# Kernel tuning notes

Hardware: AMD Instinct MI355X
Metric: run time of the kernel (lower is better)

Reference implementation:

```python
import jax, jax.numpy as jnp
import numpy as np

K = 8192  # num_embeddings
D = 256   # embedding_dim


def setup_inputs() -> dict:
    key = jax.random.key(0)
    k1, k2 = jax.random.split(key)
    z_e = jax.random.normal(k1, (16, 2048, D), dtype=jnp.float32)
    # codebook init: randn * 1/sqrt(D), matching the torch buffer init
    embedding = jax.random.normal(k2, (K, D), dtype=jnp.float32) * (1.0 / np.sqrt(D))
    return {"z_e": z_e, "embedding": embedding}


def reference(z_e, embedding):
    # Eval-mode forward of VectorQuantizerEMA (no EMA buffer update, no mask).
    B, M, Dd = z_e.shape
    Kk = embedding.shape[0]
    flat = z_e.reshape(-1, Dd)  # [N, D]

    distances = (
        jnp.sum(flat * flat, axis=1, keepdims=True)
        - 2.0 * (flat @ embedding.T)
        + jnp.sum(embedding * embedding, axis=1)[None, :]
    )
    indices = jnp.argmin(distances, axis=1)  # [N] int

    z_q = embedding[indices].reshape(B, M, Dd)
    z_q_st = z_e + jax.lax.stop_gradient(z_q - z_e)

    # instantaneous usage stats (perplexity, dead ratio)
    usage = jnp.zeros((Kk,), dtype=jnp.float32).at[indices].add(1.0)
    total = jnp.maximum(usage.sum(), 1.0)
    probs = usage / total
    safe_p = jnp.where(probs > 0, probs, 1.0)
    perplexity = jnp.exp(-jnp.sum(probs * jnp.log(safe_p)))
    dead_ratio = jnp.mean((usage == 0).astype(jnp.float32))
    stats = jnp.stack([perplexity, dead_ratio])

    return z_q_st, z_q, indices.reshape(B, M), stats
```

## Files before the change

### kernel.cpp

```cpp
#include <hip/hip_runtime.h>

#define N_ROWS 32768
#define D_DIM  256
#define K_CODES 8192

#define OUT0_OFF 0
#define OUT1_OFF 8388608
#define OUTI_OFF 16777216
#define OUTS_OFF 16809984

typedef _Float16 half4 __attribute__((ext_vector_type(4)));
typedef _Float16 half8 __attribute__((ext_vector_type(8)));
typedef float    f32x16 __attribute__((ext_vector_type(16)));

#define HN_OFF  0x400000
#define CAND_OFF 0x500000

#define MARGIN 0.05f

__global__ __launch_bounds__(256) void vq_conv_e(const float* __restrict__ E,
                                                 char* __restrict__ Estg,
                                                 float* __restrict__ hn,
                                                 int* __restrict__ usage) {
    const int wv = threadIdx.x >> 6;
    const int l = threadIdx.x & 63;
    const int code = blockIdx.x * 4 + wv;
    float4 v = ((const float4*)E)[code * 64 + l];

    const int g = code >> 6, c = code & 63;
    const int st = l >> 5;
    const int dg = ((4 * l) & 127) >> 3;
    const int slot = (dg + c) & 15;
    const int sub = 8 * (l & 1);

    half4 hh = {(_Float16)v.x, (_Float16)v.y, (_Float16)v.z, (_Float16)v.w};
    char* p = Estg + (size_t)g * 32768 + st * 16384 + c * 256 + slot * 16 + sub;
    *(half4*)p = hh;

    float s = v.x * v.x + v.y * v.y + v.z * v.z + v.w * v.w;
    #pragma unroll
    for (int off = 32; off >= 1; off >>= 1) s += __shfl_down(s, off);
    if (l == 0) hn[code] = -0.5f * s;

    if (blockIdx.x < K_CODES / 256) usage[blockIdx.x * 256 + threadIdx.x] = 0;
}

__global__ __launch_bounds__(256) void vq_conv_x(const float* __restrict__ x,
                                                 char* __restrict__ Xh) {
    const size_t i4 = ((size_t)blockIdx.x * 256 + threadIdx.x) * 4;
    float4 v = *(const float4*)(x + i4);
    half4 hh = {(_Float16)v.x, (_Float16)v.y, (_Float16)v.z, (_Float16)v.w};
    *(half4*)(Xh + i4 * 2) = hh;
}

#define STAGE_COMPUTE(LDSOFF, KSB)                                             \
    _Pragma("unroll")                                                          \
    for (int ks = 0; ks < 8; ++ks) {                                           \
        const int slot = (2 * ks + hc) & 15;                                   \
        const int sa = rb0 + slot * 16 + (LDSOFF);                             \
        half8 a0 = *(const half8*)(lds + sa);                                  \
        half8 a1 = *(const half8*)(lds + sa + 8192);                           \
        const half8 b0 = xr0[(KSB) + ks];                                      \
        const half8 b1 = xr1[(KSB) + ks];                                      \
        acc00 = __builtin_amdgcn_mfma_f32_32x32x16_f16(a0, b0, acc00, 0, 0, 0);\
        acc01 = __builtin_amdgcn_mfma_f32_32x32x16_f16(a0, b1, acc01, 0, 0, 0);\
        acc10 = __builtin_amdgcn_mfma_f32_32x32x16_f16(a1, b0, acc10, 0, 0, 0);\
        acc11 = __builtin_amdgcn_mfma_f32_32x32x16_f16(a1, b1, acc11, 0, 0, 0);\
    }

#define ISSUE_STAGE(gsrc, BUFOFF)                                              \
    _Pragma("unroll") for (int i = 0; i < 4; ++i)                              \
        __builtin_amdgcn_global_load_lds(                                      \
            (const __attribute__((address_space(1))) void*)((gsrc) + i * 4096 + t16), \
            (__attribute__((address_space(3))) void*)(lds + (BUFOFF) + i * 4096 + t16), \
            16, 0, 0);

#define TOP2_UPD(v, cidx, T0, T1, I0, I1)                                      \
    if ((v) > (T1)) {                                                          \
        const bool g_ = (v) > (T0);                                            \
        (T1) = g_ ? (T0) : (v);                                                \
        (I1) = g_ ? (I0) : (cidx);                                             \
        if (g_) { (T0) = (v); (I0) = (cidx); }                                 \
    }

__global__ __launch_bounds__(256, 2) void vq_mfma(const char* __restrict__ Estg,
                                                  const float* __restrict__ hnp,
                                                  const char* __restrict__ Xh,
                                                  float2* __restrict__ cand) {
    __shared__ __attribute__((aligned(16))) char lds[32768];

    const int tid = threadIdx.x;
    const int w = tid >> 6, lane = tid & 63;
    const int cl = lane & 31, half = lane >> 5;
    const int t16 = tid * 16;
    const int rb0 = cl * 256;
    const int hc = half + cl;

    const int part = blockIdx.x & 3;
    const int qb = blockIdx.x >> 2;
    const char* Ebase = Estg + (size_t)part * 32 * 32768;

    const int qw = qb * 256 + w * 64;
    const char* xbA = Xh + (size_t)(qw + cl) * 512 + half * 16;
    const char* xbB = Xh + (size_t)(qw + 32 + cl) * 512 + half * 16;
    half8 xr0[16], xr1[16];
    #pragma unroll
    for (int ks = 0; ks < 16; ++ks) {
        xr0[ks] = *(const half8*)(xbA + ks * 32);
        xr1[ks] = *(const half8*)(xbB + ks * 32);
    }

    ISSUE_STAGE(Ebase, 0)

    float t0a = -3.4e38f, t1a = -3.4e38f, t0b = -3.4e38f, t1b = -3.4e38f;
    int i0a = 0, i1a = 0, i0b = 0, i1b = 0;

    for (int g = 0; g < 32; ++g) {
        const char* egrp = Ebase + (size_t)g * 32768;
        const char* enxt = Ebase + (size_t)((g + 1) & 31) * 32768;

        f32x16 acc00 = {}, acc01 = {}, acc10 = {}, acc11 = {};

        __syncthreads();
        ISSUE_STAGE(egrp + 16384, 16384)
        const float* hq = hnp + part * 2048 + g * 64 + 4 * half;
        float4 hn0[4], hn1[4];
        #pragma unroll
        for (int j = 0; j < 4; ++j) {
            hn0[j] = *(const float4*)(hq + 8 * j);
            hn1[j] = *(const float4*)(hq + 32 + 8 * j);
        }
        STAGE_COMPUTE(0, 0)

        __syncthreads();
        ISSUE_STAGE(enxt, 0)
        STAGE_COMPUTE(16384, 8)

        const int gb = g * 64 + 4 * half;
        #pragma unroll
        for (int r = 0; r < 16; ++r) {
            const int rc = (r & 3) + 8 * (r >> 2);
            const float h0 = hn0[r >> 2][r & 3];
            const float h1 = hn1[r >> 2][r & 3];
            const int c0 = gb + rc, c1 = gb + 32 + rc;
            float v;
            v = acc00[r] + h0; TOP2_UPD(v, c0, t0a, t1a, i0a, i1a);
            v = acc10[r] + h1; TOP2_UPD(v, c1, t0a, t1a, i0a, i1a);
            v = acc01[r] + h0; TOP2_UPD(v, c0, t0b, t1b, i0b, i1b);
            v = acc11[r] + h1; TOP2_UPD(v, c1, t0b, t1b, i0b, i1b);
        }
    }

    const size_t bA = (size_t)(qw + cl) * 16 + part * 4 + half * 2;
    cand[bA]     = make_float2(t0a, __int_as_float(part * 2048 + i0a));
    cand[bA + 1] = make_float2(t1a, __int_as_float(part * 2048 + i1a));
    const size_t bB = (size_t)(qw + 32 + cl) * 16 + part * 4 + half * 2;
    cand[bB]     = make_float2(t0b, __int_as_float(part * 2048 + i0b));
    cand[bB + 1] = make_float2(t1b, __int_as_float(part * 2048 + i1b));
}

__global__ __launch_bounds__(64) void vq_resolve(const float2* __restrict__ cand,
                                                 const float* __restrict__ x,
                                                 const float* __restrict__ E,
                                                 float* __restrict__ outI,
                                                 int* __restrict__ wsIdx,
                                                 int* __restrict__ usage) {
    const int row = blockIdx.x;
    const int lane = threadIdx.x;

    float v = -3.4e38f;
    int ci = 0x7fffffff;
    if (lane < 16) {
        float2 c = cand[(size_t)row * 16 + lane];
        v = c.x;
        ci = __float_as_int(c.y);
    }
    float m = v;
    #pragma unroll
    for (int off = 8; off >= 1; off >>= 1) m = fmaxf(m, __shfl_xor(m, off, 16));
    m = __shfl(m, 0);

    const bool im = (lane < 16) && (v >= m - MARGIN);
    const unsigned long long mk = __ballot(im);
    int besti;
    if (__popcll(mk) == 1) {
        int wmin = im ? ci : 0x7fffffff;
        #pragma unroll
        for (int off = 8; off >= 1; off >>= 1)
            wmin = min(wmin, __shfl_xor(wmin, off, 16));
        besti = __shfl(wmin, 0);
    } else {
        const float4 x4 = *(const float4*)(x + (size_t)row * 256 + lane * 4);
        double bq = -1.0e300;
        besti = 0x7fffffff;
        unsigned long long mm = mk;
        while (mm) {
            const int j = __ffsll(mm) - 1;
            mm &= mm - 1;
            const int cidx = __shfl(ci, j);
            const float4 e4 = *(const float4*)(E + (size_t)cidx * 256 + lane * 4);
            double ps = (double)x4.x * e4.x + (double)x4.y * e4.y +
                        (double)x4.z * e4.z + (double)x4.w * e4.w -
                        0.5 * ((double)e4.x * e4.x + (double)e4.y * e4.y +
                               (double)e4.z * e4.z + (double)e4.w * e4.w);
            #pragma unroll
            for (int off = 32; off >= 1; off >>= 1) ps += __shfl_xor(ps, off);
            if (ps > bq || (ps == bq && cidx < besti)) { bq = ps; besti = cidx; }
        }
    }

    if (lane == 0) {
        outI[row] = (float)besti;
        wsIdx[row] = besti;
        atomicAdd(&usage[besti], 1);
    }
}

__global__ __launch_bounds__(64) void vq_gather(const int* __restrict__ wsIdx,
                                                const float* __restrict__ E,
                                                float* __restrict__ out0,
                                                float* __restrict__ out1) {
    const int row = blockIdx.x;
    const int lane = threadIdx.x;
    const int idx = wsIdx[row];
    float4 e4 = ((const float4*)(E + (size_t)idx * D_DIM))[lane];
    ((float4*)(out0 + (size_t)row * D_DIM))[lane] = e4;
    ((float4*)(out1 + (size_t)row * D_DIM))[lane] = e4;
}

__global__ __launch_bounds__(256) void vq_stats(const int* __restrict__ usage,
                                                float* __restrict__ statsOut) {
    __shared__ float redp[256];
    __shared__ int   redz[256];
    const int t = threadIdx.x;
    float pl = 0.0f;
    int zc = 0;
    for (int i = t; i < K_CODES; i += 256) {
        const int u = usage[i];
        if (u == 0) {
            zc++;
        } else {
            const float p = (float)u * (1.0f / (float)N_ROWS);
            pl += p * logf(p);
        }
    }
    redp[t] = pl;
    redz[t] = zc;
    __syncthreads();
    for (int s = 128; s > 0; s >>= 1) {
        if (t < s) { redp[t] += redp[t + s]; redz[t] += redz[t + s]; }
        __syncthreads();
    }
    if (t == 0) {
        statsOut[0] = expf(-redp[0]);
        statsOut[1] = (float)redz[0] / (float)K_CODES;
    }
}

extern "C" void kernel_launch(void* const* d_in, const int* in_sizes, int n_in,
                              void* d_out, int out_size, void* d_ws, size_t ws_size,
                              hipStream_t stream) {
    const float* z_e = (const float*)d_in[0];
    const float* E   = (const float*)d_in[1];

    float* out   = (float*)d_out;
    char*  out_b = (char*)d_out;

    char*   Estg  = out_b;
    float*  hn    = (float*)(out_b + HN_OFF);
    float2* candb = (float2*)(out_b + CAND_OFF);
    char*   Xh    = out_b + (size_t)OUT1_OFF * 4;

    float* out0 = out + OUT0_OFF;
    float* out1 = out + OUT1_OFF;
    float* outI = out + OUTI_OFF;
    float* outS = out + OUTS_OFF;

    int* usage = (int*)d_ws;
    int* wsIdx = (int*)((char*)d_ws + 32768);

    vq_conv_e<<<dim3(K_CODES / 4), dim3(256), 0, stream>>>(E, Estg, hn, usage);
    vq_conv_x<<<dim3(8192), dim3(256), 0, stream>>>(z_e, Xh);
    vq_mfma<<<dim3(512), dim3(256), 0, stream>>>(Estg, hn, Xh, candb);
    vq_resolve<<<dim3(N_ROWS), dim3(64), 0, stream>>>(candb, z_e, E, outI, wsIdx, usage);
    vq_gather<<<dim3(N_ROWS), dim3(64), 0, stream>>>(wsIdx, E, out0, out1);
    vq_stats<<<dim3(1), dim3(256), 0, stream>>>(usage, outS);
}
```

Measured before the change: 285.2 us.

## Fuse conversion kernels, pack group ids into low mantissa bits for argmax, widen blocks

The two conversion kernels are merged into one launch. In the MFMA kernel, the per-element top-2 tracking in the hot loop is replaced by a per-register running max: the group id is packed into the low 6 mantissa bits so fmaxf carries the index. Top-2 selection is done once after the loop. The resolve, gather and stats kernels get larger blocks with several rows per block. The packing drops precision in the low bits and keeps only one candidate per accumulator slot, which leans on the resolve margin to stay correct.

```diff
diff --git a/kernel.cpp b/kernel.cpp
--- a/kernel.cpp
+++ b/kernel.cpp
@@ -18,39 +18,42 @@
 
 #define MARGIN 0.05f
 
-__global__ __launch_bounds__(256) void vq_conv_e(const float* __restrict__ E,
-                                                 char* __restrict__ Estg,
-                                                 float* __restrict__ hn,
-                                                 int* __restrict__ usage) {
-    const int wv = threadIdx.x >> 6;
-    const int l = threadIdx.x & 63;
-    const int code = blockIdx.x * 4 + wv;
-    float4 v = ((const float4*)E)[code * 64 + l];
-
-    const int g = code >> 6, c = code & 63;
-    const int st = l >> 5;
-    const int dg = ((4 * l) & 127) >> 3;
-    const int slot = (dg + c) & 15;
-    const int sub = 8 * (l & 1);
-
-    half4 hh = {(_Float16)v.x, (_Float16)v.y, (_Float16)v.z, (_Float16)v.w};
-    char* p = Estg + (size_t)g * 32768 + st * 16384 + c * 256 + slot * 16 + sub;
-    *(half4*)p = hh;
-
-    float s = v.x * v.x + v.y * v.y + v.z * v.z + v.w * v.w;
-    #pragma unroll
-    for (int off = 32; off >= 1; off >>= 1) s += __shfl_down(s, off);
-    if (l == 0) hn[code] = -0.5f * s;
-
-    if (blockIdx.x < K_CODES / 256) usage[blockIdx.x * 256 + threadIdx.x] = 0;
-}
-
-__global__ __launch_bounds__(256) void vq_conv_x(const float* __restrict__ x,
-                                                 char* __restrict__ Xh) {
-    const size_t i4 = ((size_t)blockIdx.x * 256 + threadIdx.x) * 4;
-    float4 v = *(const float4*)(x + i4);
-    half4 hh = {(_Float16)v.x, (_Float16)v.y, (_Float16)v.z, (_Float16)v.w};
-    *(half4*)(Xh + i4 * 2) = hh;
+#define PK(v, id) __uint_as_float((__float_as_uint(v) & 0xFFFFFFC0u) | (unsigned)(id))
+
+__global__ __launch_bounds__(256) void vq_conv(const float* __restrict__ E,
+                                               const float* __restrict__ x,
+                                               char* __restrict__ Estg,
+                                               float* __restrict__ hn,
+                                               char* __restrict__ Xh,
+                                               int* __restrict__ usage) {
+    if (blockIdx.x < 2048) {
+        const int wv = threadIdx.x >> 6;
+        const int l = threadIdx.x & 63;
+        const int code = blockIdx.x * 4 + wv;
+        float4 v = ((const float4*)E)[code * 64 + l];
+
+        const int g = code >> 6, c = code & 63;
+        const int st = l >> 5;
+        const int dg = ((4 * l) & 127) >> 3;
+        const int slot = (dg + c) & 15;
+        const int sub = 8 * (l & 1);
+
+        half4 hh = {(_Float16)v.x, (_Float16)v.y, (_Float16)v.z, (_Float16)v.w};
+        char* p = Estg + (size_t)g * 32768 + st * 16384 + c * 256 + slot * 16 + sub;
+        *(half4*)p = hh;
+
+        float s = v.x * v.x + v.y * v.y + v.z * v.z + v.w * v.w;
+        #pragma unroll
+        for (int off = 32; off >= 1; off >>= 1) s += __shfl_down(s, off);
+        if (l == 0) hn[code] = -0.5f * s;
+
+        if (blockIdx.x < K_CODES / 256) usage[blockIdx.x * 256 + threadIdx.x] = 0;
+    } else {
+        const size_t i4 = ((size_t)(blockIdx.x - 2048) * 256 + threadIdx.x) * 4;
+        float4 v = *(const float4*)(x + i4);
+        half4 hh = {(_Float16)v.x, (_Float16)v.y, (_Float16)v.z, (_Float16)v.w};
+        *(half4*)(Xh + i4 * 2) = hh;
+    }
 }
 
 #define STAGE_COMPUTE(LDSOFF, KSB)                                             \
@@ -112,8 +115,9 @@
 
     ISSUE_STAGE(Ebase, 0)
 
-    float t0a = -3.4e38f, t1a = -3.4e38f, t0b = -3.4e38f, t1b = -3.4e38f;
-    int i0a = 0, i1a = 0, i0b = 0, i1b = 0;
+    float mA[16], mB[16];
+    #pragma unroll
+    for (int r = 0; r < 16; ++r) { mA[r] = -3.4e38f; mB[r] = -3.4e38f; }
 
     for (int g = 0; g < 32; ++g) {
         const char* egrp = Ebase + (size_t)g * 32768;
@@ -136,18 +140,36 @@
         ISSUE_STAGE(enxt, 0)
         STAGE_COMPUTE(16384, 8)
 
-        const int gb = g * 64 + 4 * half;
+        const int gid2 = g * 2;
         #pragma unroll
         for (int r = 0; r < 16; ++r) {
-            const int rc = (r & 3) + 8 * (r >> 2);
             const float h0 = hn0[r >> 2][r & 3];
             const float h1 = hn1[r >> 2][r & 3];
-            const int c0 = gb + rc, c1 = gb + 32 + rc;
-            float v;
-            v = acc00[r] + h0; TOP2_UPD(v, c0, t0a, t1a, i0a, i1a);
-            v = acc10[r] + h1; TOP2_UPD(v, c1, t0a, t1a, i0a, i1a);
-            v = acc01[r] + h0; TOP2_UPD(v, c0, t0b, t1b, i0b, i1b);
-            v = acc11[r] + h1; TOP2_UPD(v, c1, t0b, t1b, i0b, i1b);
+            mA[r] = fmaxf(fmaxf(mA[r], PK(acc00[r] + h0, gid2)),
+                          PK(acc10[r] + h1, gid2 + 1));
+            mB[r] = fmaxf(fmaxf(mB[r], PK(acc01[r] + h0, gid2)),
+                          PK(acc11[r] + h1, gid2 + 1));
+        }
+    }
+
+    float t0a = -3.4e38f, t1a = -3.4e38f, t0b = -3.4e38f, t1b = -3.4e38f;
+    int i0a = 0, i1a = 0, i0b = 0, i1b = 0;
+    #pragma unroll
+    for (int r = 0; r < 16; ++r) {
+        const int rc = (r & 3) + 8 * (r >> 2);
+        {
+            const unsigned b = __float_as_uint(mA[r]);
+            const int id = (int)(b & 63u);
+            const int code = (id >> 1) * 64 + (id & 1) * 32 + 4 * half + rc;
+            const float v = mA[r];
+            TOP2_UPD(v, code, t0a, t1a, i0a, i1a);
+        }
+        {
+            const unsigned b = __float_as_uint(mB[r]);
+            const int id = (int)(b & 63u);
+            const int code = (id >> 1) * 64 + (id & 1) * 32 + 4 * half + rc;
+            const float v = mB[r];
+            TOP2_UPD(v, code, t0b, t1b, i0b, i1b);
         }
     }
 
@@ -159,14 +181,14 @@
     cand[bB + 1] = make_float2(t1b, __int_as_float(part * 2048 + i1b));
 }
 
-__global__ __launch_bounds__(64) void vq_resolve(const float2* __restrict__ cand,
-                                                 const float* __restrict__ x,
-                                                 const float* __restrict__ E,
-                                                 float* __restrict__ outI,
-                                                 int* __restrict__ wsIdx,
-                                                 int* __restrict__ usage) {
-    const int row = blockIdx.x;
-    const int lane = threadIdx.x;
+__global__ __launch_bounds__(256) void vq_resolve(const float2* __restrict__ cand,
+                                                  const float* __restrict__ x,
+                                                  const float* __restrict__ E,
+                                                  float* __restrict__ outI,
+                                                  int* __restrict__ wsIdx,
+                                                  int* __restrict__ usage) {
+    const int row = blockIdx.x * 4 + (threadIdx.x >> 6);
+    const int lane = threadIdx.x & 63;
 
     float v = -3.4e38f;
     int ci = 0x7fffffff;
@@ -216,26 +238,26 @@
     }
 }
 
-__global__ __launch_bounds__(64) void vq_gather(const int* __restrict__ wsIdx,
-                                                const float* __restrict__ E,
-                                                float* __restrict__ out0,
-                                                float* __restrict__ out1) {
-    const int row = blockIdx.x;
-    const int lane = threadIdx.x;
+__global__ __launch_bounds__(256) void vq_gather(const int* __restrict__ wsIdx,
+                                                 const float* __restrict__ E,
+                                                 float* __restrict__ out0,
+                                                 float* __restrict__ out1) {
+    const int row = blockIdx.x * 4 + (threadIdx.x >> 6);
+    const int lane = threadIdx.x & 63;
     const int idx = wsIdx[row];
     float4 e4 = ((const float4*)(E + (size_t)idx * D_DIM))[lane];
     ((float4*)(out0 + (size_t)row * D_DIM))[lane] = e4;
     ((float4*)(out1 + (size_t)row * D_DIM))[lane] = e4;
 }
 
-__global__ __launch_bounds__(256) void vq_stats(const int* __restrict__ usage,
-                                                float* __restrict__ statsOut) {
-    __shared__ float redp[256];
-    __shared__ int   redz[256];
+__global__ __launch_bounds__(1024) void vq_stats(const int* __restrict__ usage,
+                                                 float* __restrict__ statsOut) {
+    __shared__ float redp[1024];
+    __shared__ int   redz[1024];
     const int t = threadIdx.x;
     float pl = 0.0f;
     int zc = 0;
-    for (int i = t; i < K_CODES; i += 256) {
+    for (int i = t; i < K_CODES; i += 1024) {
         const int u = usage[i];
         if (u == 0) {
             zc++;
@@ -247,7 +269,7 @@
     redp[t] = pl;
     redz[t] = zc;
     __syncthreads();
-    for (int s = 128; s > 0; s >>= 1) {
+    for (int s = 512; s > 0; s >>= 1) {
         if (t < s) { redp[t] += redp[t + s]; redz[t] += redz[t + s]; }
         __syncthreads();
     }
@@ -279,10 +301,9 @@
     int* usage = (int*)d_ws;
     int* wsIdx = (int*)((char*)d_ws + 32768);
 
-    vq_conv_e<<<dim3(K_CODES / 4), dim3(256), 0, stream>>>(E, Estg, hn, usage);
-    vq_conv_x<<<dim3(8192), dim3(256), 0, stream>>>(z_e, Xh);
+    vq_conv<<<dim3(10240), dim3(256), 0, stream>>>(E, z_e, Estg, hn, Xh, usage);
     vq_mfma<<<dim3(512), dim3(256), 0, stream>>>(Estg, hn, Xh, candb);
-    vq_resolve<<<dim3(N_ROWS), dim3(64), 0, stream>>>(candb, z_e, E, outI, wsIdx, usage);
-    vq_gather<<<dim3(N_ROWS), dim3(64), 0, stream>>>(wsIdx, E, out0, out1);
-    vq_stats<<<dim3(1), dim3(256), 0, stream>>>(usage, outS);
-}
+    vq_resolve<<<dim3(8192), dim3(256), 0, stream>>>(candb, z_e, E, outI, wsIdx, usage);
+    vq_gather<<<dim3(8192), dim3(256), 0, stream>>>(wsIdx, E, out0, out1);
+    vq_stats<<<dim3(1), dim3(1024), 0, stream>>>(usage, outS);
+}
```

Measured after the change: 272.4 us. 1.05x faster.
